# Kernel tuning notes

Hardware: AMD Instinct MI355X
Metric: run time of the kernel (lower is better)

Reference implementation:

```python
import jax, jax.numpy as jnp
import numpy as np
from jax import lax

BN_EPS = 1e-5

def conv_bn_prelu(x, w, b, scale, bias, a):
    # Conv2d(k=3, pad=1, stride=1) in NCHW / OIHW layout
    y = lax.conv_general_dilated(x, w, window_strides=(1, 1), padding='SAME',
                                 dimension_numbers=('NCHW', 'OIHW', 'NCHW'))
    y = y + b[None, :, None, None]
    # BatchNorm2d, training-mode batch statistics over (B, H, W)
    mean = jnp.mean(y, axis=(0, 2, 3), keepdims=True)
    var = jnp.var(y, axis=(0, 2, 3), keepdims=True)
    y = (y - mean) * lax.rsqrt(var + BN_EPS)
    y = y * scale[None, :, None, None] + bias[None, :, None, None]
    # PReLU with single shared slope parameter
    return jnp.where(y >= 0, y, a * y)

def setup_inputs() -> dict:
    key = jax.random.key(0)
    ks = jax.random.split(key, 7)
    B, C, H, W = 4, 64, 64, 64
    x = jax.random.normal(ks[0], (B, C, H, W), dtype=jnp.float32)
    conv_w = jax.random.normal(ks[1], (C, C, 3, 3), dtype=jnp.float32) * 0.05
    conv_b = jax.random.normal(ks[2], (C,), dtype=jnp.float32) * 0.05
    bn_scale = jax.random.uniform(ks[3], (C,), dtype=jnp.float32, minval=0.5, maxval=1.5)
    bn_bias = jax.random.normal(ks[4], (C,), dtype=jnp.float32) * 0.05
    prelu_a = jnp.full((1,), 0.25, dtype=jnp.float32)
    gamma = jax.random.normal(ks[5], (1,), dtype=jnp.float32)
    return {'x': x, 'conv_w': conv_w, 'conv_b': conv_b, 'bn_scale': bn_scale,
            'bn_bias': bn_bias, 'prelu_a': prelu_a, 'gamma': gamma}

def reference(x, conv_w, conv_b, bn_scale, bn_bias, prelu_a, gamma):
    B, C, H, W = x.shape
    N = H * W
    feat = conv_bn_prelu(x, conv_w, conv_b, bn_scale, bn_bias, prelu_a)  # (B,C,H,W)
    f = feat.reshape(B, C, N)  # proj_query = f^T, proj_key = f, proj_value = f
    # energy[b,i,j] = sum_c f[b,c,i] * f[b,c,j]  -> (B, N, N)
    energy = jnp.einsum('bci,bcj->bij', f, f)
    # energy_new = rowmax - energy, softmax over last dim
    energy_new = jnp.max(energy, axis=-1, keepdims=True) - energy
    attn = jax.nn.softmax(energy_new, axis=-1)
    # out = bmm(proj_value, attention^T): out[b,c,i] = sum_j f[b,c,j] * attn[b,i,j]
    out = jnp.einsum('bcj,bij->bci', f, attn).reshape(B, C, H, W)
    return gamma * out + feat
```

## Files before the change

kernel.cpp:

```cpp
#include <hip/hip_runtime.h>

constexpr int kB = 4, kC = 64, kH = 64, kW = 64, kN = kH * kW;
constexpr float kEps = 1e-5f;
constexpr int SPLIT = 4;
constexpr float kQS = 1.2011224087864498f;

#if __has_builtin(__builtin_amdgcn_exp2f)
#define EXP2F(x) __builtin_amdgcn_exp2f(x)
#else
#define EXP2F(x) exp2f(x)
#endif

typedef __attribute__((ext_vector_type(8))) short short8;
typedef __attribute__((ext_vector_type(4))) float f32x4;
typedef unsigned short u16;

__device__ inline unsigned pkbf(float a, float b) {
  unsigned ua = __float_as_uint(a), ub = __float_as_uint(b);
  ua += 0x7fff + ((ua >> 16) & 1);
  ub += 0x7fff + ((ub >> 16) & 1);
  return (ua >> 16) | (ub & 0xffff0000u);
}

__global__ __launch_bounds__(256) void prep_w_kernel(const float* __restrict__ w,
                                                     u16* __restrict__ wA,
                                                     float* __restrict__ stat) {
  if (blockIdx.x == 0) {
    stat[threadIdx.x] = 0.f;
    stat[256 + threadIdx.x] = 0.f;
  }
  int idx = blockIdx.x * 256 + threadIdx.x;
  if (idx < 64 * 576) {
    int oc = idx / 576, r = idx - oc * 576;
    int khw = r >> 6, ic = r & 63;
    float v = w[(oc * 64 + ic) * 9 + khw];
    unsigned u = __float_as_uint(v);
    u += 0x7fff + ((u >> 16) & 1);
    wA[idx] = (u16)(u >> 16);
  }
}

__global__ __launch_bounds__(256) void conv_kernel(const float* __restrict__ x,
                                                   const u16* __restrict__ wA,
                                                   const float* __restrict__ bias,
                                                   float* __restrict__ y,
                                                   float* __restrict__ stat) {
  const int tid = threadIdx.x;
  const int lane = tid & 63;
  const int wv = tid >> 6;
  const int bx = blockIdx.x;
  const int b = bx >> 7;
  const int h = (bx & 127) >> 1;
  const int w0 = (bx & 1) * 32;
  const int lw = lane & 15, lg = lane >> 4;

  __shared__ __align__(16) u16 xt[3 * 40 * 64];

#pragma unroll
  for (int rep = 0; rep < 4; ++rep) {
    int idx = rep * 256 + tid;
    if (idx < 960) {
      int kh = idx / 320;
      int t = idx - kh * 320;
      int gw = t >> 5, icp = t & 31;
      int wb = w0 - 4 + gw * 4;
      int hh = h + kh - 1;
      float4 va = {0.f, 0.f, 0.f, 0.f}, vb = {0.f, 0.f, 0.f, 0.f};
      if (hh >= 0 && hh < 64 && wb >= 0 && wb < 64) {
        va = *(const float4*)&x[((b * 64 + icp * 2) * 64 + hh) * 64 + wb];
        vb = *(const float4*)&x[((b * 64 + icp * 2 + 1) * 64 + hh) * 64 + wb];
      }
      float av[4] = {va.x, va.y, va.z, va.w};
      float bv[4] = {vb.x, vb.y, vb.z, vb.w};
#pragma unroll
      for (int j = 0; j < 4; ++j) {
        int wc = gw * 4 + j;
        *(unsigned*)&xt[(kh * 40 + wc) * 64 + (((icp >> 2) ^ (wc & 7)) * 8 + (icp & 3) * 2)] =
            pkbf(av[j], bv[j]);
      }
    }
  }
  __syncthreads();

  const int oc0 = wv * 16;
  short8 af[18];
#pragma unroll
  for (int kc = 0; kc < 18; ++kc)
    af[kc] = *(const short8*)&wA[(oc0 + lw) * 576 + kc * 32 + lg * 8];

  f32x4 acc[2];
  acc[0] = (f32x4){0.f, 0.f, 0.f, 0.f};
  acc[1] = (f32x4){0.f, 0.f, 0.f, 0.f};
#pragma unroll
  for (int kc = 0; kc < 18; ++kc) {
    const int khw = kc >> 1;
    const int kh = khw / 3, kwv = khw % 3;
#pragma unroll
    for (int nt = 0; nt < 2; ++nt) {
      int wc = nt * 16 + lw + kwv + 3;
      short8 bf = *(const short8*)&xt[(kh * 40 + wc) * 64 + ((((kc & 1) * 4 + lg) ^ (wc & 7)) * 8)];
      acc[nt] = __builtin_amdgcn_mfma_f32_16x16x32_bf16(af[kc], bf, acc[nt], 0, 0, 0);
    }
  }

  float* st = stat + (bx & 3) * 128;
#pragma unroll
  for (int r = 0; r < 4; ++r) {
    const int oc = oc0 + lg * 4 + r;
    const float bz = bias[oc];
    float v0 = acc[0][r] + bz;
    float v1 = acc[1][r] + bz;
    y[((b * 64 + oc) * 64 + h) * 64 + w0 + lw] = v0;
    y[((b * 64 + oc) * 64 + h) * 64 + w0 + 16 + lw] = v1;
    float s = v0 + v1, q = v0 * v0 + v1 * v1;
#pragma unroll
    for (int m = 1; m < 16; m <<= 1) {
      s += __shfl_xor(s, m);
      q += __shfl_xor(q, m);
    }
    if (lw == 0) {
      atomicAdd(&st[oc], s);
      atomicAdd(&st[64 + oc], q);
    }
  }
}

__global__ __launch_bounds__(256) void pack_kernel(const float* __restrict__ y,
                                                   const float* __restrict__ stat,
                                                   const float* __restrict__ scale,
                                                   const float* __restrict__ bias,
                                                   const float* __restrict__ pa,
                                                   float* __restrict__ ABg,
                                                   u16* __restrict__ fbfA,
                                                   u16* __restrict__ fbfB) {
  __shared__ float ls[64 * 65];
  __shared__ float sAB[128];
  const int tid = threadIdx.x;
  const int b = blockIdx.x >> 6;
  const int n0 = (blockIdx.x & 63) << 6;
  if (tid < 64) {
    const float inv_n = 1.f / (float)(kB * kN);
    float ssum = stat[tid] + stat[128 + tid] + stat[256 + tid] + stat[384 + tid];
    float qsum = stat[64 + tid] + stat[192 + tid] + stat[320 + tid] + stat[448 + tid];
    float mean = ssum * inv_n;
    float var = qsum * inv_n - mean * mean;
    float A = scale[tid] * rsqrtf(var + kEps);
    float Bc = bias[tid] - mean * A;
    sAB[tid] = A;
    sAB[64 + tid] = Bc;
    ABg[tid] = A;
    ABg[64 + tid] = Bc;
  }
  __syncthreads();
  {
    const int c = tid >> 2, nj = (tid & 3) << 4;
    const float A = sAB[c], Bc = sAB[64 + c], a = pa[0];
    const float* yp = y + ((b * kC + c) * kN) + n0 + nj;
    float f[16];
#pragma unroll
    for (int v = 0; v < 4; ++v) {
      float4 xv = *(const float4*)(yp + v * 4);
      float t;
      t = fmaf(A, xv.x, Bc); f[v * 4 + 0] = t >= 0.f ? t : a * t;
      t = fmaf(A, xv.y, Bc); f[v * 4 + 1] = t >= 0.f ? t : a * t;
      t = fmaf(A, xv.z, Bc); f[v * 4 + 2] = t >= 0.f ? t : a * t;
      t = fmaf(A, xv.w, Bc); f[v * 4 + 3] = t >= 0.f ? t : a * t;
    }
#pragma unroll
    for (int v = 0; v < 16; ++v) ls[c * 65 + nj + v] = f[v];
  }
  __syncthreads();
  {
    int chunk = tid >> 5, pt = chunk >> 1, kc = chunk & 1;
    int lp2 = (tid & 31) * 2;
    u16* dst = fbfA + ((size_t)((b * 256 + (n0 >> 4) + pt) * 2 + kc)) * 512;
#pragma unroll
    for (int e = 0; e < 2; ++e) {
      int L = lp2 + e;
      int n = pt * 16 + (L & 15);
      int cb = kc * 32 + (L >> 4) * 8;
      float v[8];
#pragma unroll
      for (int r = 0; r < 8; ++r) v[r] = kQS * ls[(cb + r) * 65 + n];
      uint4 o = {pkbf(v[0], v[1]), pkbf(v[2], v[3]), pkbf(v[4], v[5]), pkbf(v[6], v[7])};
      *(uint4*)&dst[L * 8] = o;
    }
  }
  {
    int chunk = tid >> 5, jt = chunk >> 2, ct = chunk & 3;
    int lp2 = (tid & 31) * 2;
    u16* dst = fbfB + ((size_t)((b * 128 + (n0 >> 5) + jt) * 4 + ct)) * 512;
#pragma unroll
    for (int e = 0; e < 2; ++e) {
      int L = lp2 + e;
      int c = ct * 16 + (L & 15);
      int nb = jt * 32 + (L >> 4) * 8;
      float v[8];
#pragma unroll
      for (int r = 0; r < 8; ++r) v[r] = ls[c * 65 + nb + r];
      uint4 o = {pkbf(v[0], v[1]), pkbf(v[2], v[3]), pkbf(v[4], v[5]), pkbf(v[6], v[7])};
      *(uint4*)&dst[L * 8] = o;
    }
  }
}

__global__ __launch_bounds__(512, 1) void attn_kernel(const u16* __restrict__ fbfA,
                                                      const u16* __restrict__ fbfB,
                                                      float* __restrict__ Op,
                                                      float* __restrict__ lp) {
  const int tid = threadIdx.x;
  const int lane = tid & 63;
  const int w = tid >> 6;
  const int wq = w & 3, jh = w >> 2;
  const int bx = blockIdx.x;
  const int s = bx & 3, itb = (bx >> 2) & 15, b = bx >> 6;
  const int c15 = lane & 15, g = lane >> 4;

  __shared__ __align__(16) float RedU[20480];
  u16* ps = (u16*)RedU + w * 2560;
  const int pw_off = c15 * 40 + g * 4;
  const int pr_off = c15 * 40 + g * 8;

  const uint4* fA = (const uint4*)fbfA;
  const uint4* fB = (const uint4*)fbfB;

  uint4 qf[4][2];
  const int ptq = itb * 16 + wq * 4;
#pragma unroll
  for (int it = 0; it < 4; ++it)
#pragma unroll
    for (int kc = 0; kc < 2; ++kc) {
      uint4 q = fA[(size_t)((b * 256 + ptq + it) * 2 + kc) * 64 + lane];
      q.x ^= 0x80008000u; q.y ^= 0x80008000u; q.z ^= 0x80008000u; q.w ^= 0x80008000u;
      qf[it][kc] = q;
    }

  const short8 ones = {0x3F80, 0x3F80, 0x3F80, 0x3F80, 0x3F80, 0x3F80, 0x3F80, 0x3F80};

  f32x4 oacc[4][4];
  f32x4 lacc[4];
#pragma unroll
  for (int it = 0; it < 4; ++it) {
    lacc[it] = (f32x4){0.f, 0.f, 0.f, 0.f};
#pragma unroll
    for (int ct = 0; ct < 4; ++ct) oacc[it][ct] = (f32x4){0.f, 0.f, 0.f, 0.f};
  }

#pragma unroll 2
  for (int jj2 = 0; jj2 < 16; ++jj2) {
    const int jj = jj2 * 2 + jh;
    const int j0 = (s * 32 + jj) * 32;
    const int ca = (b * 256 + (j0 >> 4)) * 2;
    uint4 a00 = fA[(size_t)(ca + 0) * 64 + lane];
    uint4 a01 = fA[(size_t)(ca + 1) * 64 + lane];
    uint4 a10 = fA[(size_t)(ca + 2) * 64 + lane];
    uint4 a11 = fA[(size_t)(ca + 3) * 64 + lane];
    const int cb = (b * 128 + (j0 >> 5)) * 4;
    uint4 v0 = fB[(size_t)(cb + 0) * 64 + lane];
    uint4 v1 = fB[(size_t)(cb + 1) * 64 + lane];
    uint4 v2 = fB[(size_t)(cb + 2) * 64 + lane];
    uint4 v3 = fB[(size_t)(cb + 3) * 64 + lane];

    f32x4 sv[2][4];
#pragma unroll
    for (int it = 0; it < 4; ++it) {
      f32x4 z0 = (f32x4){0.f, 0.f, 0.f, 0.f};
      z0 = __builtin_amdgcn_mfma_f32_16x16x32_bf16(*(short8*)&a00, *(short8*)&qf[it][0], z0, 0, 0, 0);
      z0 = __builtin_amdgcn_mfma_f32_16x16x32_bf16(*(short8*)&a01, *(short8*)&qf[it][1], z0, 0, 0, 0);
      sv[0][it] = z0;
      f32x4 z1 = (f32x4){0.f, 0.f, 0.f, 0.f};
      z1 = __builtin_amdgcn_mfma_f32_16x16x32_bf16(*(short8*)&a10, *(short8*)&qf[it][0], z1, 0, 0, 0);
      z1 = __builtin_amdgcn_mfma_f32_16x16x32_bf16(*(short8*)&a11, *(short8*)&qf[it][1], z1, 0, 0, 0);
      sv[1][it] = z1;
    }
#pragma unroll
    for (int it = 0; it < 4; ++it)
#pragma unroll
      for (int jt = 0; jt < 2; ++jt) {
        float p0 = EXP2F(sv[jt][it][0]);
        float p1 = EXP2F(sv[jt][it][1]);
        float p2 = EXP2F(sv[jt][it][2]);
        float p3 = EXP2F(sv[jt][it][3]);
        uint2 d;
        d.x = __builtin_amdgcn_perm(__float_as_uint(p1), __float_as_uint(p0), 0x07060302u);
        d.y = __builtin_amdgcn_perm(__float_as_uint(p3), __float_as_uint(p2), 0x07060302u);
        *(uint2*)&ps[pw_off + it * 640 + jt * 16] = d;
      }
#pragma unroll
    for (int it = 0; it < 4; ++it) {
      short8 pf = *(const short8*)&ps[pr_off + it * 640];
      lacc[it] = __builtin_amdgcn_mfma_f32_16x16x32_bf16(pf, ones, lacc[it], 0, 0, 0);
      oacc[it][0] = __builtin_amdgcn_mfma_f32_16x16x32_bf16(pf, *(short8*)&v0, oacc[it][0], 0, 0, 0);
      oacc[it][1] = __builtin_amdgcn_mfma_f32_16x16x32_bf16(pf, *(short8*)&v1, oacc[it][1], 0, 0, 0);
      oacc[it][2] = __builtin_amdgcn_mfma_f32_16x16x32_bf16(pf, *(short8*)&v2, oacc[it][2], 0, 0, 0);
      oacc[it][3] = __builtin_amdgcn_mfma_f32_16x16x32_bf16(pf, *(short8*)&v3, oacc[it][3], 0, 0, 0);
    }
  }

  __syncthreads();
  if (jh == 1) {
    float* dst = RedU + wq * 5120;
#pragma unroll
    for (int it = 0; it < 4; ++it)
#pragma unroll
      for (int ct = 0; ct < 4; ++ct)
        *(f32x4*)&dst[(it * 4 + ct) * 256 + lane * 4] = oacc[it][ct];
#pragma unroll
    for (int it = 0; it < 4; ++it)
      *(f32x4*)&dst[(16 + it) * 256 + lane * 4] = lacc[it];
  }
  __syncthreads();
  if (jh == 0) {
    const float* src = RedU + wq * 5120;
#pragma unroll
    for (int it = 0; it < 4; ++it) {
#pragma unroll
      for (int ct = 0; ct < 4; ++ct)
        oacc[it][ct] = oacc[it][ct] + *(const f32x4*)&src[(it * 4 + ct) * 256 + lane * 4];
      lacc[it] = lacc[it] + *(const f32x4*)&src[(16 + it) * 256 + lane * 4];
    }

    const int rbase = (s * kB + b) * kN + itb * 256 + wq * 64;
    float* Ow = Op + (size_t)rbase * 64;
#pragma unroll
    for (int it = 0; it < 4; ++it)
#pragma unroll
      for (int ct = 0; ct < 4; ++ct)
#pragma unroll
        for (int r = 0; r < 4; ++r)
          Ow[(it * 16 + g * 4 + r) * 64 + ct * 16 + c15] = oacc[it][ct][r];
    if (c15 == 0) {
      float* lw_ = lp + rbase;
#pragma unroll
      for (int it = 0; it < 4; ++it)
#pragma unroll
        for (int r = 0; r < 4; ++r) lw_[it * 16 + g * 4 + r] = lacc[it][r];
    }
  }
}

__global__ __launch_bounds__(256) void combine_kernel(const float* __restrict__ Op,
                                                      const float* __restrict__ lp,
                                                      const float* __restrict__ y,
                                                      const float* __restrict__ ABg,
                                                      const float* __restrict__ pa,
                                                      const float* __restrict__ gamma_p,
                                                      float* __restrict__ out) {
  const int tid = threadIdx.x;
  const int bx = blockIdx.x;
  const int b = bx >> 6, it64 = bx & 63;
  const int i0 = it64 * 64;
  __shared__ float tr[64 * 65];
  __shared__ float linv[64];
  if (tid < 64) {
    float sum = 0.f;
    for (int s = 0; s < SPLIT; ++s) sum += lp[(size_t)(s * kB + b) * kN + i0 + tid];
    linv[tid] = 1.f / sum;
  }
  __syncthreads();
  const float gm = gamma_p[0];
  const float a = pa[0];
#pragma unroll
  for (int rr = 0; rr < 4; ++rr) {
    int flat4 = rr * 256 + tid;
    int i = flat4 >> 4, c4 = (flat4 & 15) * 4;
    float4 acc = {0.f, 0.f, 0.f, 0.f};
    for (int s = 0; s < SPLIT; ++s) {
      float4 v = *(const float4*)&Op[((size_t)(s * kB + b) * kN + i0 + i) * 64 + c4];
      acc.x += v.x; acc.y += v.y; acc.z += v.z; acc.w += v.w;
    }
    float sc = gm * linv[i];
    tr[(c4 + 0) * 65 + i] = acc.x * sc;
    tr[(c4 + 1) * 65 + i] = acc.y * sc;
    tr[(c4 + 2) * 65 + i] = acc.z * sc;
    tr[(c4 + 3) * 65 + i] = acc.w * sc;
  }
  __syncthreads();
#pragma unroll
  for (int rr = 0; rr < 4; ++rr) {
    int flat4 = rr * 256 + tid;
    int c = flat4 >> 4, i4 = (flat4 & 15) * 4;
    const float A = ABg[c], Bc = ABg[64 + c];
    float4 yv = *(const float4*)&y[(size_t)(b * 64 + c) * 4096 + it64 * 64 + i4];
    float t;
    float4 ov;
    t = fmaf(A, yv.x, Bc); t = t >= 0.f ? t : a * t; ov.x = tr[c * 65 + i4 + 0] + t;
    t = fmaf(A, yv.y, Bc); t = t >= 0.f ? t : a * t; ov.y = tr[c * 65 + i4 + 1] + t;
    t = fmaf(A, yv.z, Bc); t = t >= 0.f ? t : a * t; ov.z = tr[c * 65 + i4 + 2] + t;
    t = fmaf(A, yv.w, Bc); t = t >= 0.f ? t : a * t; ov.w = tr[c * 65 + i4 + 3] + t;
    *(float4*)&out[(size_t)(b * 64 + c) * 4096 + it64 * 64 + i4] = ov;
  }
}

extern "C" void kernel_launch(void* const* d_in, const int* in_sizes, int n_in,
                              void* d_out, int out_size, void* d_ws, size_t ws_size,
                              hipStream_t stream) {
  (void)in_sizes; (void)n_in; (void)out_size; (void)ws_size;
  const float* x        = (const float*)d_in[0];
  const float* conv_w   = (const float*)d_in[1];
  const float* conv_b   = (const float*)d_in[2];
  const float* bn_scale = (const float*)d_in[3];
  const float* bn_bias  = (const float*)d_in[4];
  const float* prelu_a  = (const float*)d_in[5];
  const float* gamma    = (const float*)d_in[6];
  float* out = (float*)d_out;

  u16* fbfA = (u16*)d_ws;
  u16* fbfB = fbfA + kB * kC * kN;
  float* stat = (float*)(fbfB + kB * kC * kN);
  float* ABg = stat + 512;
  u16* wA = (u16*)(ABg + 128);
  float* Op = (float*)(wA + 36864);
  float* lp = Op + (size_t)SPLIT * kB * kN * 64;

  float* y = out;

  prep_w_kernel<<<144, 256, 0, stream>>>(conv_w, wA, stat);
  conv_kernel<<<kB * kH * 2, 256, 0, stream>>>(x, wA, conv_b, y, stat);
  pack_kernel<<<kB * (kN / 64), 256, 0, stream>>>(y, stat, bn_scale, bn_bias, prelu_a,
                                                  ABg, fbfA, fbfB);
  attn_kernel<<<kB * 16 * SPLIT, 512, 0, stream>>>(fbfA, fbfB, Op, lp);
  combine_kernel<<<kB * 64, 256, 0, stream>>>(Op, lp, y, ABg, prelu_a, gamma, out);
}
```

Baseline: 123.9 us.

## Fuse combine into attention kernel via in-block split-K reduction over eight waves

```diff
diff --git a/kernel.cpp b/kernel.cpp
--- a/kernel.cpp
+++ b/kernel.cpp
@@ -2,7 +2,6 @@
 
 constexpr int kB = 4, kC = 64, kH = 64, kW = 64, kN = kH * kW;
 constexpr float kEps = 1e-5f;
-constexpr int SPLIT = 4;
 constexpr float kQS = 1.2011224087864498f;
 
 #if __has_builtin(__builtin_amdgcn_exp2f)
@@ -206,18 +205,20 @@
 
 __global__ __launch_bounds__(512, 1) void attn_kernel(const u16* __restrict__ fbfA,
                                                       const u16* __restrict__ fbfB,
-                                                      float* __restrict__ Op,
-                                                      float* __restrict__ lp) {
+                                                      const float* y,
+                                                      const float* __restrict__ ABg,
+                                                      const float* __restrict__ pa,
+                                                      const float* __restrict__ gamma_p,
+                                                      float* out) {
   const int tid = threadIdx.x;
   const int lane = tid & 63;
   const int w = tid >> 6;
-  const int wq = w & 3, jh = w >> 2;
   const int bx = blockIdx.x;
-  const int s = bx & 3, itb = (bx >> 2) & 15, b = bx >> 6;
+  const int b = bx >> 6, it4 = bx & 63;
   const int c15 = lane & 15, g = lane >> 4;
 
-  __shared__ __align__(16) float RedU[20480];
-  u16* ps = (u16*)RedU + w * 2560;
+  __shared__ __align__(16) float Red[20480];
+  u16* ps = (u16*)Red + w * 2560;
   const int pw_off = c15 * 40 + g * 4;
   const int pr_off = c15 * 40 + g * 8;
 
@@ -225,12 +226,11 @@
   const uint4* fB = (const uint4*)fbfB;
 
   uint4 qf[4][2];
-  const int ptq = itb * 16 + wq * 4;
 #pragma unroll
   for (int it = 0; it < 4; ++it)
 #pragma unroll
     for (int kc = 0; kc < 2; ++kc) {
-      uint4 q = fA[(size_t)((b * 256 + ptq + it) * 2 + kc) * 64 + lane];
+      uint4 q = fA[(size_t)((b * 256 + it4 * 4 + it) * 2 + kc) * 64 + lane];
       q.x ^= 0x80008000u; q.y ^= 0x80008000u; q.z ^= 0x80008000u; q.w ^= 0x80008000u;
       qf[it][kc] = q;
     }
@@ -248,14 +248,13 @@
 
 #pragma unroll 2
   for (int jj2 = 0; jj2 < 16; ++jj2) {
-    const int jj = jj2 * 2 + jh;
-    const int j0 = (s * 32 + jj) * 32;
-    const int ca = (b * 256 + (j0 >> 4)) * 2;
+    const int jj = jj2 * 8 + w;
+    const int ca = (b * 256 + jj * 2) * 2;
     uint4 a00 = fA[(size_t)(ca + 0) * 64 + lane];
     uint4 a01 = fA[(size_t)(ca + 1) * 64 + lane];
     uint4 a10 = fA[(size_t)(ca + 2) * 64 + lane];
     uint4 a11 = fA[(size_t)(ca + 3) * 64 + lane];
-    const int cb = (b * 128 + (j0 >> 5)) * 4;
+    const int cb = (b * 128 + jj) * 4;
     uint4 v0 = fB[(size_t)(cb + 0) * 64 + lane];
     uint4 v1 = fB[(size_t)(cb + 1) * 64 + lane];
     uint4 v2 = fB[(size_t)(cb + 2) * 64 + lane];
@@ -297,98 +296,63 @@
     }
   }
 
+  for (int half = 4; half >= 1; half >>= 1) {
+    __syncthreads();
+    if (w >= half && w < 2 * half) {
+      float* dst = Red + (w - half) * 5120;
+#pragma unroll
+      for (int it = 0; it < 4; ++it) {
+#pragma unroll
+        for (int ct = 0; ct < 4; ++ct)
+          *(f32x4*)&dst[(it * 4 + ct) * 256 + lane * 4] = oacc[it][ct];
+        *(f32x4*)&dst[(16 + it) * 256 + lane * 4] = lacc[it];
+      }
+    }
+    __syncthreads();
+    if (w < half) {
+      const float* src = Red + w * 5120;
+#pragma unroll
+      for (int it = 0; it < 4; ++it) {
+#pragma unroll
+        for (int ct = 0; ct < 4; ++ct)
+          oacc[it][ct] = oacc[it][ct] + *(const f32x4*)&src[(it * 4 + ct) * 256 + lane * 4];
+        lacc[it] = lacc[it] + *(const f32x4*)&src[(16 + it) * 256 + lane * 4];
+      }
+    }
+  }
+
+  float* tr = Red + 5120;
+  if (w == 0) {
+    const float gm = gamma_p[0];
+#pragma unroll
+    for (int it = 0; it < 4; ++it) {
+      f32x4 sc;
+#pragma unroll
+      for (int r = 0; r < 4; ++r) sc[r] = gm / lacc[it][r];
+#pragma unroll
+      for (int ct = 0; ct < 4; ++ct)
+#pragma unroll
+        for (int r = 0; r < 4; ++r)
+          tr[(ct * 16 + c15) * 65 + it * 16 + g * 4 + r] = oacc[it][ct][r] * sc[r];
+    }
+  }
   __syncthreads();
-  if (jh == 1) {
-    float* dst = RedU + wq * 5120;
-#pragma unroll
-    for (int it = 0; it < 4; ++it)
-#pragma unroll
-      for (int ct = 0; ct < 4; ++ct)
-        *(f32x4*)&dst[(it * 4 + ct) * 256 + lane * 4] = oacc[it][ct];
-#pragma unroll
-    for (int it = 0; it < 4; ++it)
-      *(f32x4*)&dst[(16 + it) * 256 + lane * 4] = lacc[it];
-  }
-  __syncthreads();
-  if (jh == 0) {
-    const float* src = RedU + wq * 5120;
-#pragma unroll
-    for (int it = 0; it < 4; ++it) {
-#pragma unroll
-      for (int ct = 0; ct < 4; ++ct)
-        oacc[it][ct] = oacc[it][ct] + *(const f32x4*)&src[(it * 4 + ct) * 256 + lane * 4];
-      lacc[it] = lacc[it] + *(const f32x4*)&src[(16 + it) * 256 + lane * 4];
-    }
-
-    const int rbase = (s * kB + b) * kN + itb * 256 + wq * 64;
-    float* Ow = Op + (size_t)rbase * 64;
-#pragma unroll
-    for (int it = 0; it < 4; ++it)
-#pragma unroll
-      for (int ct = 0; ct < 4; ++ct)
-#pragma unroll
-        for (int r = 0; r < 4; ++r)
-          Ow[(it * 16 + g * 4 + r) * 64 + ct * 16 + c15] = oacc[it][ct][r];
-    if (c15 == 0) {
-      float* lw_ = lp + rbase;
-#pragma unroll
-      for (int it = 0; it < 4; ++it)
-#pragma unroll
-        for (int r = 0; r < 4; ++r) lw_[it * 16 + g * 4 + r] = lacc[it][r];
-    }
-  }
-}
-
-__global__ __launch_bounds__(256) void combine_kernel(const float* __restrict__ Op,
-                                                      const float* __restrict__ lp,
-                                                      const float* __restrict__ y,
-                                                      const float* __restrict__ ABg,
-                                                      const float* __restrict__ pa,
-                                                      const float* __restrict__ gamma_p,
-                                                      float* __restrict__ out) {
-  const int tid = threadIdx.x;
-  const int bx = blockIdx.x;
-  const int b = bx >> 6, it64 = bx & 63;
-  const int i0 = it64 * 64;
-  __shared__ float tr[64 * 65];
-  __shared__ float linv[64];
-  if (tid < 64) {
-    float sum = 0.f;
-    for (int s = 0; s < SPLIT; ++s) sum += lp[(size_t)(s * kB + b) * kN + i0 + tid];
-    linv[tid] = 1.f / sum;
-  }
-  __syncthreads();
-  const float gm = gamma_p[0];
+
   const float a = pa[0];
 #pragma unroll
-  for (int rr = 0; rr < 4; ++rr) {
-    int flat4 = rr * 256 + tid;
-    int i = flat4 >> 4, c4 = (flat4 & 15) * 4;
-    float4 acc = {0.f, 0.f, 0.f, 0.f};
-    for (int s = 0; s < SPLIT; ++s) {
-      float4 v = *(const float4*)&Op[((size_t)(s * kB + b) * kN + i0 + i) * 64 + c4];
-      acc.x += v.x; acc.y += v.y; acc.z += v.z; acc.w += v.w;
-    }
-    float sc = gm * linv[i];
-    tr[(c4 + 0) * 65 + i] = acc.x * sc;
-    tr[(c4 + 1) * 65 + i] = acc.y * sc;
-    tr[(c4 + 2) * 65 + i] = acc.z * sc;
-    tr[(c4 + 3) * 65 + i] = acc.w * sc;
-  }
-  __syncthreads();
-#pragma unroll
-  for (int rr = 0; rr < 4; ++rr) {
-    int flat4 = rr * 256 + tid;
+  for (int rr = 0; rr < 2; ++rr) {
+    int flat4 = rr * 512 + tid;
     int c = flat4 >> 4, i4 = (flat4 & 15) * 4;
     const float A = ABg[c], Bc = ABg[64 + c];
-    float4 yv = *(const float4*)&y[(size_t)(b * 64 + c) * 4096 + it64 * 64 + i4];
+    const size_t idx = (size_t)(b * 64 + c) * 4096 + it4 * 64 + i4;
+    float4 yv = *(const float4*)&y[idx];
     float t;
     float4 ov;
     t = fmaf(A, yv.x, Bc); t = t >= 0.f ? t : a * t; ov.x = tr[c * 65 + i4 + 0] + t;
     t = fmaf(A, yv.y, Bc); t = t >= 0.f ? t : a * t; ov.y = tr[c * 65 + i4 + 1] + t;
     t = fmaf(A, yv.z, Bc); t = t >= 0.f ? t : a * t; ov.z = tr[c * 65 + i4 + 2] + t;
     t = fmaf(A, yv.w, Bc); t = t >= 0.f ? t : a * t; ov.w = tr[c * 65 + i4 + 3] + t;
-    *(float4*)&out[(size_t)(b * 64 + c) * 4096 + it64 * 64 + i4] = ov;
+    *(float4*)&out[idx] = ov;
   }
 }
 
@@ -410,8 +374,6 @@
   float* stat = (float*)(fbfB + kB * kC * kN);
   float* ABg = stat + 512;
   u16* wA = (u16*)(ABg + 128);
-  float* Op = (float*)(wA + 36864);
-  float* lp = Op + (size_t)SPLIT * kB * kN * 64;
 
   float* y = out;
 
@@ -419,6 +381,5 @@
   conv_kernel<<<kB * kH * 2, 256, 0, stream>>>(x, wA, conv_b, y, stat);
   pack_kernel<<<kB * (kN / 64), 256, 0, stream>>>(y, stat, bn_scale, bn_bias, prelu_a,
                                                   ABg, fbfA, fbfB);
-  attn_kernel<<<kB * 16 * SPLIT, 512, 0, stream>>>(fbfA, fbfB, Op, lp);
-  combine_kernel<<<kB * 64, 256, 0, stream>>>(Op, lp, y, ABg, prelu_a, gamma, out);
-}
+  attn_kernel<<<kB * 64, 512, 0, stream>>>(fbfA, fbfB, y, ABg, prelu_a, gamma, out);
+}
```

Result: faster. 115.8 us (-6.5%).
